# Performance work log

Hardware: AMD Instinct MI355X
Metric: run time of the kernel (lower is better)

Reference implementation:

```python
import jax, jax.numpy as jnp
import numpy as np

HEAD_DIM = 128
NEG = -1e9


def setup_inputs() -> dict:
    key = jax.random.key(0)
    kq, kk, kv, kl = jax.random.split(key, 4)
    B, S, D = 8, 2048, HEAD_DIM
    q = jax.random.normal(kq, (B, S, D), dtype=jnp.float32)
    k = jax.random.normal(kk, (B, S, D), dtype=jnp.float32)
    v = jax.random.normal(kv, (B, S, D), dtype=jnp.float32)
    event_length = jax.random.randint(kl, (B,), 0, 2048, dtype=jnp.int32)
    return {"q": q, "k": k, "v": v, "event_length": event_length}


def reference(q, k, v, event_length):
    B, S, D = q.shape
    scale = jnp.sqrt(jnp.asarray(D, dtype=q.dtype))
    # [B, S, S] attention scores
    scores = jnp.einsum("bsd,btd->bst", q, k) / scale
    idx = jnp.arange(S)
    valid = idx[None, :] < event_length[:, None]          # [B, S]
    mask = valid[:, :, None] & valid[:, None, :]          # [B, S, S]
    scores = jnp.where(mask, scores, jnp.asarray(NEG, dtype=scores.dtype))
    attn = jax.nn.softmax(scores, axis=-1)
    # dropout is eval-mode identity
    return jnp.einsum("bst,btd->bsd", attn, v)
```

## Files before the change

kernel.cpp:

```cpp
#include <hip/hip_runtime.h>

#define S 2048
#define D 128
#define BATCH 8
#define NS 4
#define KSTR 136
#define VSTR 72

typedef _Float16 half8 __attribute__((ext_vector_type(8)));
typedef _Float16 half4_t __attribute__((ext_vector_type(4)));
typedef float f4 __attribute__((ext_vector_type(4)));

__device__ __forceinline__ half8 cvt8(f4 a, f4 b) {
    half8 h;
    h[0] = (_Float16)a[0]; h[1] = (_Float16)a[1];
    h[2] = (_Float16)a[2]; h[3] = (_Float16)a[3];
    h[4] = (_Float16)b[0]; h[5] = (_Float16)b[1];
    h[6] = (_Float16)b[2]; h[7] = (_Float16)b[3];
    return h;
}

__global__ __launch_bounds__(256) void k_prep(const float* __restrict__ kin,
                                              const float* __restrict__ v,
                                              _Float16* __restrict__ kh,
                                              _Float16* __restrict__ vt,
                                              float* __restrict__ psums,
                                              unsigned* __restrict__ done) {
    int b = blockIdx.y, c = blockIdx.x, tid = threadIdx.x;
    if (b == 0 && c == 0 && tid < 256) done[tid] = 0u;
    size_t off = ((size_t)b * S + c * 64) * D;
    #pragma unroll
    for (int p = 0; p < 4; ++p) {
        size_t i = (size_t)p * 2048 + tid * 8;
        f4 a = *(const f4*)(kin + off + i);
        f4 bb = *(const f4*)(kin + off + i + 4);
        *(half8*)(kh + off + i) = cvt8(a, bb);
    }
    __shared__ float tile[64 * 132];
    __shared__ f4 sred[256][2];
    f4 a0 = {0.f, 0.f, 0.f, 0.f}, a1 = {0.f, 0.f, 0.f, 0.f};
    int d0 = (tid & 15) * 8;
    #pragma unroll
    for (int p = 0; p < 4; ++p) {
        int t = p * 16 + (tid >> 4);
        f4 x = *(const f4*)(v + off + (size_t)t * D + d0);
        f4 y = *(const f4*)(v + off + (size_t)t * D + d0 + 4);
        a0 += x; a1 += y;
        *(f4*)&tile[t * 132 + d0] = x;
        *(f4*)&tile[t * 132 + d0 + 4] = y;
    }
    sred[tid][0] = a0; sred[tid][1] = a1;
    __syncthreads();
    if (tid < 16) {
        f4 s0 = sred[tid][0], s1 = sred[tid][1];
        for (int g = 1; g < 16; ++g) { s0 += sred[g * 16 + tid][0]; s1 += sred[g * 16 + tid][1]; }
        *(f4*)(psums + (b * 32 + c) * 128 + tid * 8) = s0;
        *(f4*)(psums + (b * 32 + c) * 128 + tid * 8 + 4) = s1;
    }
    int u = tid & 7, dd = tid >> 3;
    #pragma unroll
    for (int pass = 0; pass < 4; ++pass) {
        int d = pass * 32 + dd;
        half8 h;
        #pragma unroll
        for (int i = 0; i < 8; ++i) h[i] = (_Float16)tile[(u * 8 + i) * 132 + d];
        *(half8*)(vt + ((size_t)(b * D + d)) * S + c * 64 + u * 8) = h;
    }
}

__global__ __launch_bounds__(256, 3) void k_attn(
    const float* __restrict__ q, const _Float16* __restrict__ kh,
    const _Float16* __restrict__ vt, const int* __restrict__ el,
    const float* __restrict__ psums, _Float16* __restrict__ part,
    float* __restrict__ stats, unsigned* __restrict__ done,
    float* __restrict__ out) {
    int nm[BATCH], fm[BATCH], T = 0, F = 0;
    #pragma unroll
    for (int bb = 0; bb < BATCH; ++bb) {
        int g = (el[bb] + 63) >> 6;
        nm[bb] = g * NS; T += g * NS;
        fm[bb] = 32 - g; F += 32 - g;
    }
    int it = blockIdx.x, tid = threadIdx.x;
    __shared__ float cmean[128];
    __shared__ int cflag;

    if (it >= T) {
        if (it >= T + F) return;
        int rel = it - T, b = 0;
        while (rel >= fm[b]) { rel -= fm[b]; ++b; }
        int mg = ((el[b] + 63) >> 6) + rel;
        int m0 = mg * 64;
        if (tid < 128) {
            float cs = 0.f;
            #pragma unroll 4
            for (int cc = 0; cc < 32; ++cc) cs += psums[(b * 32 + cc) * 128 + tid];
            cmean[tid] = cs * (1.0f / (float)S);
        }
        __syncthreads();
        int d0 = (tid & 31) * 4, r0 = tid >> 5;
        f4 mv = *(const f4*)&cmean[d0];
        #pragma unroll
        for (int i = 0; i < 8; ++i) {
            int row = m0 + r0 + 8 * i;
            *(f4*)(out + ((size_t)b * S + row) * D + d0) = mv;
        }
        return;
    }

    int rel = it, b = 0;
    while (rel >= nm[b]) { rel -= nm[b]; ++b; }
    int mg = rel >> 2, j = rel & 3;
    int Lb = el[b], m0 = mg * 64;
    int nkt = (Lb + 63) >> 6;

    int lane = tid & 63, w = tid >> 6;
    int col = lane & 15, quad = lane >> 4;

    __shared__ _Float16 Kh[64 * KSTR];
    __shared__ _Float16 Vt[128 * VSTR];

    const float scale = 0.0883883476483184f;
    half8 qf[4];
    {
        const float* qb = q + ((size_t)b * S + m0 + w * 16 + col) * D;
        #pragma unroll
        for (int kc = 0; kc < 4; ++kc) {
            f4 a = *(const f4*)(qb + kc * 32 + quad * 8);
            f4 b2 = *(const f4*)(qb + kc * 32 + quad * 8 + 4);
            a *= scale; b2 *= scale;
            qf[kc] = cvt8(a, b2);
        }
    }

    f4 O[8];
    #pragma unroll
    for (int i = 0; i < 8; ++i) O[i] = (f4){0.f, 0.f, 0.f, 0.f};
    float ps = 0.f;

    int kr = tid >> 4, kc8 = (tid & 15) << 3;
    int vr = tid >> 3, vc8 = (tid & 7) << 3;
    const _Float16* kb_ = kh + (size_t)b * S * D;
    const _Float16* vb_ = vt + (size_t)b * D * S;

    if (j < nkt) {
        half8 kreg[4], vreg[4];
        {
            int t0 = j * 64;
            #pragma unroll
            for (int p = 0; p < 4; ++p)
                kreg[p] = *(const half8*)(kb_ + (size_t)(t0 + p * 16 + kr) * D + kc8);
            #pragma unroll
            for (int p = 0; p < 4; ++p)
                vreg[p] = *(const half8*)(vb_ + (size_t)(p * 32 + vr) * S + t0 + vc8);
            #pragma unroll
            for (int p = 0; p < 4; ++p)
                *(half8*)&Kh[(p * 16 + kr) * KSTR + kc8] = kreg[p];
            #pragma unroll
            for (int p = 0; p < 4; ++p)
                *(half8*)&Vt[(p * 32 + vr) * VSTR + vc8] = vreg[p];
        }
        __syncthreads();

        for (int kt = j; kt < nkt; kt += NS) {
            int t0 = kt * 64;
            bool hasnext = (kt + NS) < nkt;
            if (hasnext) {
                int tn = t0 + NS * 64;
                #pragma unroll
                for (int p = 0; p < 4; ++p)
                    kreg[p] = *(const half8*)(kb_ + (size_t)(tn + p * 16 + kr) * D + kc8);
                #pragma unroll
                for (int p = 0; p < 4; ++p)
                    vreg[p] = *(const half8*)(vb_ + (size_t)(p * 32 + vr) * S + tn + vc8);
            }
            #pragma unroll
            for (int nt = 0; nt < 4; ++nt) {
                f4 sa = {0.f, 0.f, 0.f, 0.f};
                #pragma unroll
                for (int kc = 0; kc < 4; ++kc) {
                    half8 kf = *(const half8*)&Kh[(nt * 16 + col) * KSTR + kc * 32 + quad * 8];
                    sa = __builtin_amdgcn_mfma_f32_16x16x32_f16(kf, qf[kc], sa, 0, 0, 0);
                }
                int tq = t0 + nt * 16 + quad * 4;
                half4_t ph;
                #pragma unroll
                for (int r = 0; r < 4; ++r) {
                    float e = (tq + r < Lb) ? __expf(fminf(sa[r], 10.0f)) : 0.f;
                    ps += e;
                    ph[r] = (_Float16)e;
                }
                #pragma unroll
                for (int dt = 0; dt < 8; ++dt) {
                    half4_t vf = *(const half4_t*)&Vt[(dt * 16 + col) * VSTR + nt * 16 + quad * 4];
                    O[dt] = __builtin_amdgcn_mfma_f32_16x16x16f16(ph, vf, O[dt], 0, 0, 0);
                }
            }
            if (hasnext) {
                __syncthreads();
                #pragma unroll
                for (int p = 0; p < 4; ++p)
                    *(half8*)&Kh[(p * 16 + kr) * KSTR + kc8] = kreg[p];
                #pragma unroll
                for (int p = 0; p < 4; ++p)
                    *(half8*)&Vt[(p * 32 + vr) * VSTR + vc8] = vreg[p];
                __syncthreads();
            }
        }
    }

    ps += __shfl_xor(ps, 16, 64);
    ps += __shfl_xor(ps, 32, 64);
    size_t pbase = (size_t)(j * BATCH + b) * S;
    #pragma unroll
    for (int dt = 0; dt < 8; ++dt)
        #pragma unroll
        for (int r = 0; r < 4; ++r) {
            int row = m0 + w * 16 + quad * 4 + r;
            part[(pbase + row) * D + dt * 16 + col] = (_Float16)O[dt][r];
        }
    if (quad == 0) stats[pbase + m0 + w * 16 + col] = ps;

    __syncthreads();
    if (tid == 0) {
        unsigned old = __hip_atomic_fetch_add(&done[b * 32 + mg], 1u,
                                              __ATOMIC_ACQ_REL,
                                              __HIP_MEMORY_SCOPE_AGENT);
        cflag = (old == NS - 1);
    }
    __syncthreads();
    if (!cflag) return;

    bool needMean = (Lb - m0) < 64;
    if (needMean) {
        if (tid < 128) {
            float cs = 0.f;
            #pragma unroll 4
            for (int cc = 0; cc < 32; ++cc) cs += psums[(b * 32 + cc) * 128 + tid];
            cmean[tid] = cs * (1.0f / (float)S);
        }
        __syncthreads();
    }
    int r2 = tid >> 2, d0c = (tid & 3) * 32;
    int srow = m0 + r2;
    float* orow = out + ((size_t)b * S + srow) * D + d0c;
    if (srow >= Lb) {
        #pragma unroll
        for (int sg = 0; sg < 8; ++sg)
            *(f4*)(orow + sg * 4) = *(const f4*)&cmean[d0c + sg * 4];
    } else {
        float l = 0.f;
        #pragma unroll
        for (int jj = 0; jj < NS; ++jj)
            l += stats[(size_t)(jj * BATCH + b) * S + srow];
        float inv = 1.0f / l;
        f4 o[8];
        #pragma unroll
        for (int i = 0; i < 8; ++i) o[i] = (f4){0.f, 0.f, 0.f, 0.f};
        #pragma unroll
        for (int jj = 0; jj < NS; ++jj) {
            const half8* p = (const half8*)(part + ((size_t)(jj * BATCH + b) * S + srow) * D + d0c);
            #pragma unroll
            for (int sg = 0; sg < 4; ++sg) {
                half8 h = p[sg];
                f4 x0 = {(float)h[0], (float)h[1], (float)h[2], (float)h[3]};
                f4 x1 = {(float)h[4], (float)h[5], (float)h[6], (float)h[7]};
                o[sg * 2] += x0;
                o[sg * 2 + 1] += x1;
            }
        }
        #pragma unroll
        for (int i = 0; i < 8; ++i) *(f4*)(orow + i * 4) = o[i] * inv;
    }
}

extern "C" void kernel_launch(void* const* d_in, const int* in_sizes, int n_in,
                              void* d_out, int out_size, void* d_ws, size_t ws_size,
                              hipStream_t stream) {
    const float* q = (const float*)d_in[0];
    const float* k = (const float*)d_in[1];
    const float* v = (const float*)d_in[2];
    const int* el = (const int*)d_in[3];
    float* out = (float*)d_out;

    const size_t SZ_DONE = 1024;
    const size_t SZ_PS = (size_t)BATCH * 32 * 128 * 4;
    const size_t SZ_HALF = (size_t)BATCH * D * S * 2;
    const size_t SZ_STAT = (size_t)NS * BATCH * S * 4;
    unsigned* done = (unsigned*)d_ws;
    float* psums = (float*)((char*)d_ws + SZ_DONE);
    _Float16* kh = (_Float16*)((char*)d_ws + SZ_DONE + SZ_PS);
    _Float16* vt = (_Float16*)((char*)d_ws + SZ_DONE + SZ_PS + SZ_HALF);
    float* stats = (float*)((char*)d_ws + SZ_DONE + SZ_PS + 2 * SZ_HALF);
    _Float16* part = (_Float16*)((char*)d_ws + SZ_DONE + SZ_PS + 2 * SZ_HALF + SZ_STAT);

    k_prep<<<dim3(32, 8), 256, 0, stream>>>(k, v, kh, vt, psums, done);
    k_attn<<<dim3(1024), 256, 0, stream>>>(q, kh, vt, el, psums, part, stats,
                                           done, out);
}
```

Before: 122.1 us.

## Split KV into two-tile chunks with persistent grid and separate combine kernel

Replaces the fixed four-way KV split and atomic last-block combine with a variable split in which each work item covers two 64-key tiles, so the number of chunks per query tile grows with sequence length. A grid-stride loop over 1024 blocks processes the work items, and a third kernel merges the partial outputs and row sums, which removes the done counters and atomics. Occupancy in launch_bounds rises from 3 to 4 blocks. The partial buffers grow to up to 16 chunks, and the extra launch adds traffic and overhead in exchange for better load balance.

```diff
diff --git a/kernel.cpp b/kernel.cpp
--- a/kernel.cpp
+++ b/kernel.cpp
@@ -3,9 +3,10 @@
 #define S 2048
 #define D 128
 #define BATCH 8
-#define NS 4
 #define KSTR 136
 #define VSTR 72
+#define GRID 1024
+#define MAXC 16
 
 typedef _Float16 half8 __attribute__((ext_vector_type(8)));
 typedef _Float16 half4_t __attribute__((ext_vector_type(4)));
@@ -16,7 +17,7 @@
     h[0] = (_Float16)a[0]; h[1] = (_Float16)a[1];
     h[2] = (_Float16)a[2]; h[3] = (_Float16)a[3];
     h[4] = (_Float16)b[0]; h[5] = (_Float16)b[1];
-    h[6] = (_Float16)b[2]; h[7] = (_Float16)b[3];
+    h[6] = (_Float16)b[2]; h[7] = (_Float16)b[7 - 7 + 3];
     return h;
 }
 
@@ -24,10 +25,8 @@
                                               const float* __restrict__ v,
                                               _Float16* __restrict__ kh,
                                               _Float16* __restrict__ vt,
-                                              float* __restrict__ psums,
-                                              unsigned* __restrict__ done) {
+                                              float* __restrict__ psums) {
     int b = blockIdx.y, c = blockIdx.x, tid = threadIdx.x;
-    if (b == 0 && c == 0 && tid < 256) done[tid] = 0u;
     size_t off = ((size_t)b * S + c * 64) * D;
     #pragma unroll
     for (int p = 0; p < 4; ++p) {
@@ -68,85 +67,83 @@
     }
 }
 
-__global__ __launch_bounds__(256, 3) void k_attn(
+__global__ __launch_bounds__(256, 4) void k_attn(
     const float* __restrict__ q, const _Float16* __restrict__ kh,
     const _Float16* __restrict__ vt, const int* __restrict__ el,
     const float* __restrict__ psums, _Float16* __restrict__ part,
-    float* __restrict__ stats, unsigned* __restrict__ done,
-    float* __restrict__ out) {
-    int nm[BATCH], fm[BATCH], T = 0, F = 0;
+    float* __restrict__ stats, float* __restrict__ out) {
+    int nm[BATCH], fm[BATCH], ncv[BATCH], T = 0, F = 0;
     #pragma unroll
     for (int bb = 0; bb < BATCH; ++bb) {
         int g = (el[bb] + 63) >> 6;
-        nm[bb] = g * NS; T += g * NS;
+        int nc = (g + 1) >> 1;
+        ncv[bb] = nc; nm[bb] = g * nc; T += g * nc;
         fm[bb] = 32 - g; F += 32 - g;
     }
-    int it = blockIdx.x, tid = threadIdx.x;
-    __shared__ float cmean[128];
-    __shared__ int cflag;
-
-    if (it >= T) {
-        if (it >= T + F) return;
-        int rel = it - T, b = 0;
-        while (rel >= fm[b]) { rel -= fm[b]; ++b; }
-        int mg = ((el[b] + 63) >> 6) + rel;
-        int m0 = mg * 64;
-        if (tid < 128) {
-            float cs = 0.f;
-            #pragma unroll 4
-            for (int cc = 0; cc < 32; ++cc) cs += psums[(b * 32 + cc) * 128 + tid];
-            cmean[tid] = cs * (1.0f / (float)S);
-        }
-        __syncthreads();
-        int d0 = (tid & 31) * 4, r0 = tid >> 5;
-        f4 mv = *(const f4*)&cmean[d0];
-        #pragma unroll
-        for (int i = 0; i < 8; ++i) {
-            int row = m0 + r0 + 8 * i;
-            *(f4*)(out + ((size_t)b * S + row) * D + d0) = mv;
-        }
-        return;
-    }
-
-    int rel = it, b = 0;
-    while (rel >= nm[b]) { rel -= nm[b]; ++b; }
-    int mg = rel >> 2, j = rel & 3;
-    int Lb = el[b], m0 = mg * 64;
-    int nkt = (Lb + 63) >> 6;
-
-    int lane = tid & 63, w = tid >> 6;
+    int tid = threadIdx.x, lane = tid & 63, w = tid >> 6;
     int col = lane & 15, quad = lane >> 4;
+    int kr = tid >> 4, kc8 = (tid & 15) << 3;
+    int vr = tid >> 3, vc8 = (tid & 7) << 3;
+    const float scale = 0.0883883476483184f;
 
     __shared__ _Float16 Kh[64 * KSTR];
     __shared__ _Float16 Vt[128 * VSTR];
-
-    const float scale = 0.0883883476483184f;
-    half8 qf[4];
-    {
-        const float* qb = q + ((size_t)b * S + m0 + w * 16 + col) * D;
-        #pragma unroll
-        for (int kc = 0; kc < 4; ++kc) {
-            f4 a = *(const f4*)(qb + kc * 32 + quad * 8);
-            f4 b2 = *(const f4*)(qb + kc * 32 + quad * 8 + 4);
-            a *= scale; b2 *= scale;
-            qf[kc] = cvt8(a, b2);
-        }
-    }
-
-    f4 O[8];
-    #pragma unroll
-    for (int i = 0; i < 8; ++i) O[i] = (f4){0.f, 0.f, 0.f, 0.f};
-    float ps = 0.f;
-
-    int kr = tid >> 4, kc8 = (tid & 15) << 3;
-    int vr = tid >> 3, vc8 = (tid & 7) << 3;
-    const _Float16* kb_ = kh + (size_t)b * S * D;
-    const _Float16* vb_ = vt + (size_t)b * D * S;
-
-    if (j < nkt) {
-        half8 kreg[4], vreg[4];
+    __shared__ float cmean[128];
+
+    for (int item = blockIdx.x; item < T + F; item += GRID) {
+        __syncthreads();
+
+        if (item >= T) {
+            int rel = item - T, b = 0;
+            while (rel >= fm[b]) { rel -= fm[b]; ++b; }
+            int mg = ((el[b] + 63) >> 6) + rel;
+            int m0 = mg * 64;
+            if (tid < 128) {
+                float cs = 0.f;
+                #pragma unroll 4
+                for (int cc = 0; cc < 32; ++cc) cs += psums[(b * 32 + cc) * 128 + tid];
+                cmean[tid] = cs * (1.0f / (float)S);
+            }
+            __syncthreads();
+            int d0 = (tid & 31) * 4, r0 = tid >> 5;
+            f4 mv = *(const f4*)&cmean[d0];
+            #pragma unroll
+            for (int i = 0; i < 8; ++i) {
+                int row = m0 + r0 + 8 * i;
+                *(f4*)(out + ((size_t)b * S + row) * D + d0) = mv;
+            }
+            continue;
+        }
+
+        int rel = item, b = 0;
+        while (rel >= nm[b]) { rel -= nm[b]; ++b; }
+        int nc = ncv[b];
+        int mg = rel / nc, c = rel - mg * nc;
+        int Lb = el[b], m0 = mg * 64;
+        int g = (Lb + 63) >> 6;
+        int kt0 = c * 2, t0 = kt0 * 64;
+        bool has2 = (kt0 + 1) < g;
+
+        half8 qf[4];
         {
-            int t0 = j * 64;
+            const float* qb = q + ((size_t)b * S + m0 + w * 16 + col) * D;
+            #pragma unroll
+            for (int kc = 0; kc < 4; ++kc) {
+                f4 a = *(const f4*)(qb + kc * 32 + quad * 8);
+                f4 b2 = *(const f4*)(qb + kc * 32 + quad * 8 + 4);
+                a *= scale; b2 *= scale;
+                qf[kc] = cvt8(a, b2);
+            }
+        }
+        f4 O[8];
+        #pragma unroll
+        for (int i = 0; i < 8; ++i) O[i] = (f4){0.f, 0.f, 0.f, 0.f};
+        float ps = 0.f;
+        const _Float16* kb_ = kh + (size_t)b * S * D;
+        const _Float16* vb_ = vt + (size_t)b * D * S;
+
+        {
+            half8 kreg[4], vreg[4];
             #pragma unroll
             for (int p = 0; p < 4; ++p)
                 kreg[p] = *(const half8*)(kb_ + (size_t)(t0 + p * 16 + kr) * D + kc8);
@@ -161,19 +158,31 @@
                 *(half8*)&Vt[(p * 32 + vr) * VSTR + vc8] = vreg[p];
         }
         __syncthreads();
-
-        for (int kt = j; kt < nkt; kt += NS) {
-            int t0 = kt * 64;
-            bool hasnext = (kt + NS) < nkt;
-            if (hasnext) {
-                int tn = t0 + NS * 64;
+        half8 kreg2[4], vreg2[4];
+        if (has2) {
+            int t1 = t0 + 64;
+            #pragma unroll
+            for (int p = 0; p < 4; ++p)
+                kreg2[p] = *(const half8*)(kb_ + (size_t)(t1 + p * 16 + kr) * D + kc8);
+            #pragma unroll
+            for (int p = 0; p < 4; ++p)
+                vreg2[p] = *(const half8*)(vb_ + (size_t)(p * 32 + vr) * S + t1 + vc8);
+        }
+
+        #pragma unroll
+        for (int half = 0; half < 2; ++half) {
+            if (half == 1) {
+                if (!has2) break;
+                __syncthreads();
                 #pragma unroll
                 for (int p = 0; p < 4; ++p)
-                    kreg[p] = *(const half8*)(kb_ + (size_t)(tn + p * 16 + kr) * D + kc8);
+                    *(half8*)&Kh[(p * 16 + kr) * KSTR + kc8] = kreg2[p];
                 #pragma unroll
                 for (int p = 0; p < 4; ++p)
-                    vreg[p] = *(const half8*)(vb_ + (size_t)(p * 32 + vr) * S + tn + vc8);
-            }
+                    *(half8*)&Vt[(p * 32 + vr) * VSTR + vc8] = vreg2[p];
+                __syncthreads();
+            }
+            int tb = t0 + half * 64;
             #pragma unroll
             for (int nt = 0; nt < 4; ++nt) {
                 f4 sa = {0.f, 0.f, 0.f, 0.f};
@@ -182,7 +191,7 @@
                     half8 kf = *(const half8*)&Kh[(nt * 16 + col) * KSTR + kc * 32 + quad * 8];
                     sa = __builtin_amdgcn_mfma_f32_16x16x32_f16(kf, qf[kc], sa, 0, 0, 0);
                 }
-                int tq = t0 + nt * 16 + quad * 4;
+                int tq = tb + nt * 16 + quad * 4;
                 half4_t ph;
                 #pragma unroll
                 for (int r = 0; r < 4; ++r) {
@@ -196,42 +205,30 @@
                     O[dt] = __builtin_amdgcn_mfma_f32_16x16x16f16(ph, vf, O[dt], 0, 0, 0);
                 }
             }
-            if (hasnext) {
-                __syncthreads();
-                #pragma unroll
-                for (int p = 0; p < 4; ++p)
-                    *(half8*)&Kh[(p * 16 + kr) * KSTR + kc8] = kreg[p];
-                #pragma unroll
-                for (int p = 0; p < 4; ++p)
-                    *(half8*)&Vt[(p * 32 + vr) * VSTR + vc8] = vreg[p];
-                __syncthreads();
-            }
-        }
-    }
-
-    ps += __shfl_xor(ps, 16, 64);
-    ps += __shfl_xor(ps, 32, 64);
-    size_t pbase = (size_t)(j * BATCH + b) * S;
-    #pragma unroll
-    for (int dt = 0; dt < 8; ++dt)
-        #pragma unroll
-        for (int r = 0; r < 4; ++r) {
-            int row = m0 + w * 16 + quad * 4 + r;
-            part[(pbase + row) * D + dt * 16 + col] = (_Float16)O[dt][r];
-        }
-    if (quad == 0) stats[pbase + m0 + w * 16 + col] = ps;
-
-    __syncthreads();
-    if (tid == 0) {
-        unsigned old = __hip_atomic_fetch_add(&done[b * 32 + mg], 1u,
-                                              __ATOMIC_ACQ_REL,
-                                              __HIP_MEMORY_SCOPE_AGENT);
-        cflag = (old == NS - 1);
-    }
-    __syncthreads();
-    if (!cflag) return;
-
-    bool needMean = (Lb - m0) < 64;
+        }
+
+        ps += __shfl_xor(ps, 16, 64);
+        ps += __shfl_xor(ps, 32, 64);
+        size_t pbase = (size_t)(c * BATCH + b) * S;
+        #pragma unroll
+        for (int dt = 0; dt < 8; ++dt)
+            #pragma unroll
+            for (int r = 0; r < 4; ++r) {
+                int row = m0 + w * 16 + quad * 4 + r;
+                part[(pbase + row) * D + dt * 16 + col] = (_Float16)O[dt][r];
+            }
+        if (quad == 0) stats[pbase + m0 + w * 16 + col] = ps;
+    }
+}
+
+__global__ __launch_bounds__(256) void k_comb(
+    const _Float16* __restrict__ part, const float* __restrict__ stats,
+    const float* __restrict__ psums, const int* __restrict__ el,
+    float* __restrict__ out) {
+    int b = blockIdx.y, mg = blockIdx.x, tid = threadIdx.x;
+    int L = el[b], m0 = mg * 64;
+    __shared__ float cmean[128];
+    bool needMean = (m0 + 63) >= L;
     if (needMean) {
         if (tid < 128) {
             float cs = 0.f;
@@ -241,37 +238,38 @@
         }
         __syncthreads();
     }
-    int r2 = tid >> 2, d0c = (tid & 3) * 32;
-    int srow = m0 + r2;
-    float* orow = out + ((size_t)b * S + srow) * D + d0c;
-    if (srow >= Lb) {
+    int r = tid >> 2, d0 = (tid & 3) * 32;
+    int srow = m0 + r;
+    float* orow = out + ((size_t)b * S + srow) * D + d0;
+    if (srow >= L) {
         #pragma unroll
         for (int sg = 0; sg < 8; ++sg)
-            *(f4*)(orow + sg * 4) = *(const f4*)&cmean[d0c + sg * 4];
-    } else {
-        float l = 0.f;
-        #pragma unroll
-        for (int jj = 0; jj < NS; ++jj)
-            l += stats[(size_t)(jj * BATCH + b) * S + srow];
-        float inv = 1.0f / l;
-        f4 o[8];
-        #pragma unroll
-        for (int i = 0; i < 8; ++i) o[i] = (f4){0.f, 0.f, 0.f, 0.f};
-        #pragma unroll
-        for (int jj = 0; jj < NS; ++jj) {
-            const half8* p = (const half8*)(part + ((size_t)(jj * BATCH + b) * S + srow) * D + d0c);
-            #pragma unroll
-            for (int sg = 0; sg < 4; ++sg) {
-                half8 h = p[sg];
-                f4 x0 = {(float)h[0], (float)h[1], (float)h[2], (float)h[3]};
-                f4 x1 = {(float)h[4], (float)h[5], (float)h[6], (float)h[7]};
-                o[sg * 2] += x0;
-                o[sg * 2 + 1] += x1;
-            }
-        }
-        #pragma unroll
-        for (int i = 0; i < 8; ++i) *(f4*)(orow + i * 4) = o[i] * inv;
-    }
+            *(f4*)(orow + sg * 4) = *(const f4*)&cmean[d0 + sg * 4];
+        return;
+    }
+    int g = (L + 63) >> 6;
+    int nc = (g + 1) >> 1;
+    size_t rbase = (size_t)b * S + srow;
+    const size_t step = (size_t)BATCH * S;
+    float l = 0.f;
+    for (int jj = 0; jj < nc; ++jj) l += stats[rbase + jj * step];
+    float inv = 1.0f / l;
+    f4 o[8];
+    #pragma unroll
+    for (int i = 0; i < 8; ++i) o[i] = (f4){0.f, 0.f, 0.f, 0.f};
+    for (int jj = 0; jj < nc; ++jj) {
+        const half8* p = (const half8*)(part + (rbase + jj * step) * D + d0);
+        #pragma unroll
+        for (int sg = 0; sg < 4; ++sg) {
+            half8 h = p[sg];
+            f4 x0 = {(float)h[0], (float)h[1], (float)h[2], (float)h[3]};
+            f4 x1 = {(float)h[4], (float)h[5], (float)h[6], (float)h[7]};
+            o[sg * 2] += x0;
+            o[sg * 2 + 1] += x1;
+        }
+    }
+    #pragma unroll
+    for (int i = 0; i < 8; ++i) *(f4*)(orow + i * 4) = o[i] * inv;
 }
 
 extern "C" void kernel_launch(void* const* d_in, const int* in_sizes, int n_in,
@@ -283,18 +281,16 @@
     const int* el = (const int*)d_in[3];
     float* out = (float*)d_out;
 
-    const size_t SZ_DONE = 1024;
     const size_t SZ_PS = (size_t)BATCH * 32 * 128 * 4;
     const size_t SZ_HALF = (size_t)BATCH * D * S * 2;
-    const size_t SZ_STAT = (size_t)NS * BATCH * S * 4;
-    unsigned* done = (unsigned*)d_ws;
-    float* psums = (float*)((char*)d_ws + SZ_DONE);
-    _Float16* kh = (_Float16*)((char*)d_ws + SZ_DONE + SZ_PS);
-    _Float16* vt = (_Float16*)((char*)d_ws + SZ_DONE + SZ_PS + SZ_HALF);
-    float* stats = (float*)((char*)d_ws + SZ_DONE + SZ_PS + 2 * SZ_HALF);
-    _Float16* part = (_Float16*)((char*)d_ws + SZ_DONE + SZ_PS + 2 * SZ_HALF + SZ_STAT);
-
-    k_prep<<<dim3(32, 8), 256, 0, stream>>>(k, v, kh, vt, psums, done);
-    k_attn<<<dim3(1024), 256, 0, stream>>>(q, kh, vt, el, psums, part, stats,
-                                           done, out);
-}
+    const size_t SZ_STAT = (size_t)MAXC * BATCH * S * 4;
+    float* psums = (float*)d_ws;
+    _Float16* kh = (_Float16*)((char*)d_ws + SZ_PS);
+    _Float16* vt = (_Float16*)((char*)d_ws + SZ_PS + SZ_HALF);
+    float* stats = (float*)((char*)d_ws + SZ_PS + 2 * SZ_HALF);
+    _Float16* part = (_Float16*)((char*)d_ws + SZ_PS + 2 * SZ_HALF + SZ_STAT);
+
+    k_prep<<<dim3(32, 8), 256, 0, stream>>>(k, v, kh, vt, psums);
+    k_attn<<<dim3(GRID), 256, 0, stream>>>(q, kh, vt, el, psums, part, stats, out);
+    k_comb<<<dim3(32, 8), 256, 0, stream>>>(part, stats, psums, el, out);
+}
```

After: 125.4 us. 1.03x slower.
